# Performance work log

Measured on AMD Instinct MI355X. Metric: run time of the kernel, lower is better.

The kernel has to match this reference:

```python
import jax, jax.numpy as jnp
import numpy as np


def silu(v):
    return v * jax.nn.sigmoid(v)


def setup_inputs() -> dict:
    key = jax.random.key(0)
    ks = jax.random.split(key, 10)
    b, l, d_model = 1, 1024, 1536
    d_inner, dt_rank, d_state, d_conv = 3072, 96, 16, 4
    rn = lambda k, shp, sc: jax.random.normal(k, shp, jnp.float32) * sc
    return {
        "hidden_states": rn(ks[0], (b, l, d_model), 1.0),
        "in_proj_w": rn(ks[1], (2 * d_inner, d_model), 0.02),
        "conv_w": rn(ks[2], (d_inner, d_conv), 0.1),
        "conv_b": rn(ks[3], (d_inner,), 0.1),
        "x_proj_w": rn(ks[4], (dt_rank + 2 * d_state, d_inner), 0.02),
        "dt_proj_w": rn(ks[5], (d_inner, dt_rank), 0.02),
        "dt_proj_b": rn(ks[6], (d_inner,), 0.1),
        "out_proj_w": rn(ks[7], (d_model, d_inner), 0.02),
        "A_log": jnp.log(jax.random.uniform(ks[8], (d_inner, d_state), jnp.float32, 0.5, 8.0)),
        "D": rn(ks[9], (d_inner,), 1.0),
    }


def reference(hidden_states, in_proj_w, conv_w, conv_b, x_proj_w, dt_proj_w, dt_proj_b, out_proj_w, A_log, D):
    b, l, _ = hidden_states.shape
    d_inner, d_conv = conv_w.shape
    dt_rank = dt_proj_w.shape[1]
    d_state = A_log.shape[1]
    negA = -jnp.exp(A_log)  # (d_inner, d_state)

    # in_proj, transpose to channel-major: (b, 2*d_inner, l)
    xz = jnp.einsum('bld,ed->ble', hidden_states, in_proj_w).transpose(0, 2, 1)
    x, z = jnp.split(xz, 2, axis=1)  # each (b, d_inner, l)

    # conv_state = F.pad(x, (d_conv - l, 0)) -> last d_conv columns (l > d_conv)
    conv_state = x[:, :, -d_conv:]

    # causal depthwise conv1d + bias + silu
    xp = jnp.pad(x, ((0, 0), (0, 0), (d_conv - 1, 0)))
    xc = conv_b[None, :, None] + sum(conv_w[None, :, j:j + 1] * xp[:, :, j:j + l] for j in range(d_conv))
    xc = silu(xc)  # (b, d_inner, l)

    # x_proj over channel dim -> dt, B, C
    x_dbl = jnp.einsum('bdl,ed->ble', xc, x_proj_w)  # (b, l, dt_rank+2*d_state)
    dt, Bm, Cm = jnp.split(x_dbl, [dt_rank, dt_rank + d_state], axis=-1)

    # dt_proj (no bias here; bias folded into softplus as delta_bias)
    delta = jax.nn.softplus(jnp.einsum('blr,dr->bdl', dt, dt_proj_w) + dt_proj_b[None, :, None])

    # selective scan: h_t = exp(delta_t * A) * h_{t-1} + delta_t * B_t * x_t
    deltaA = jnp.exp(delta[..., None] * negA[None, :, None, :])          # (b, d, l, n)
    deltaBx = delta[..., None] * Bm[:, None, :, :] * xc[..., None]        # (b, d, l, n)

    def comb(c1, c2):
        a1, u1 = c1
        a2, u2 = c2
        return a1 * a2, a2 * u1 + u2

    _, h = jax.lax.associative_scan(comb, (deltaA, deltaBx), axis=2)      # (b, d, l, n)

    y = jnp.einsum('bdln,bln->bdl', h, Cm) + D[None, :, None] * xc
    y = y * silu(z)

    out = jnp.einsum('bdl,od->blo', y, out_proj_w)  # (b, l, d_model)
    last_state = h[:, :, -1, :]                     # (b, d_inner, d_state)
    return out, conv_state, last_state
```

## Files before the change

kernel.cpp:

```cpp
#include <hip/hip_runtime.h>

using f32x4  = __attribute__((ext_vector_type(4))) float;
using bf16x4 = __attribute__((ext_vector_type(4))) __bf16;
using bf16x8 = __attribute__((ext_vector_type(8))) __bf16;

#define L_SEQ 1024
#define D_MODEL 1536
#define D_INNER 3072
#define DT_RANK 96
#define D_STATE 16

#define SCAN_NC 32
#define SCAN_CL (L_SEQ / SCAN_NC)
#define NCHAIN  (D_INNER * D_STATE)

#define SCRATCH_FLOATS (4 * L_SEQ * D_INNER + L_SEQ * 128 + 3 * SCAN_NC * NCHAIN)
__device__ __align__(16) float g_scratch[SCRATCH_FLOATS];

template <int BM, int BN, int BK, int AMODE, int BMODE, int EPI, int SWZY = 0>
__global__ __launch_bounds__(256) void gemm_bt(
    const float* __restrict__ Ap, const float* __restrict__ Bp,
    float* __restrict__ out0, float* __restrict__ out1,
    const float* __restrict__ bias,
    int M, int N, int K, int lda, int ldb, int ldc)
{
    constexpr int LDSK = BK + 8;
    constexpr int WM = BM / 2, WN = BN / 2;
    constexpr int FM = WM / 16, FN = WN / 16;
    constexpr int CHA = (BM * BK / 256) / 4;
    constexpr int CHB = (BN * BK / 256) / 4;
    constexpr int CPR = BK / 4;
    __shared__ __align__(16) __bf16 As [BM * LDSK];
    __shared__ __align__(16) __bf16 As2[(AMODE == 2) ? BM * LDSK : 8];
    __shared__ __align__(16) __bf16 Bs [BN * LDSK];
    __shared__ __align__(16) __bf16 Bs2[(BMODE == 2) ? BN * LDSK : 8];

    const int tid  = threadIdx.x;
    const int lane = tid & 63;
    const int wid  = tid >> 6;
    const int wm = wid >> 1, wn = wid & 1;

    int m0, n0;
    if constexpr (SWZY > 0) {
        int b   = blockIdx.x;
        int xcd = b & 7;
        int j   = b >> 3;
        m0 = (j / SWZY) * BM;
        n0 = (xcd * SWZY + (j % SWZY)) * BN;
    } else {
        m0 = blockIdx.x * BM;
        n0 = blockIdx.y * BN;
    }

    const int nkt = (K + BK - 1) / BK;
    const int per = (nkt + (int)gridDim.z - 1) / (int)gridDim.z;
    const int kb  = blockIdx.z * per * BK;
    const int ke  = min(K, kb + per * BK);

    f32x4 acc[FM][FN];
#pragma unroll
    for (int i = 0; i < FM; ++i)
#pragma unroll
        for (int j = 0; j < FN; ++j) acc[i][j] = f32x4{0.f, 0.f, 0.f, 0.f};

    const int fr = lane & 15, kq = lane >> 4;

    f32x4 arg[CHA], brg[CHB];

    auto loadA = [&](int kt) {
#pragma unroll
        for (int i = 0; i < CHA; ++i) {
            int c = i * 256 + tid;
            int r = c / CPR, k4 = c % CPR;
            arg[i] = *(const f32x4*)(Ap + (size_t)(m0 + r) * lda + kt + k4 * 4);
        }
    };
    auto loadB = [&](int kt) {
#pragma unroll
        for (int i = 0; i < CHB; ++i) {
            int c = i * 256 + tid;
            int r = c / CPR, k4 = c % CPR;
            brg[i] = *(const f32x4*)(Bp + (size_t)(n0 + r) * ldb + kt + k4 * 4);
        }
    };
    auto writeA = [&]() {
#pragma unroll
        for (int i = 0; i < CHA; ++i) {
            int c = i * 256 + tid;
            int r = c / CPR, k4 = c % CPR;
            bf16x4 hv;
#pragma unroll
            for (int e = 0; e < 4; ++e) hv[e] = (__bf16)arg[i][e];
            *(bf16x4*)&As[r * LDSK + k4 * 4] = hv;
            if constexpr (AMODE == 2) {
                bf16x4 lv;
#pragma unroll
                for (int e = 0; e < 4; ++e)
                    lv[e] = (__bf16)(arg[i][e] - (float)hv[e]);
                *(bf16x4*)&As2[r * LDSK + k4 * 4] = lv;
            }
        }
    };
    auto writeB = [&]() {
#pragma unroll
        for (int i = 0; i < CHB; ++i) {
            int c = i * 256 + tid;
            int r = c / CPR, k4 = c % CPR;
            bf16x4 hv;
#pragma unroll
            for (int e = 0; e < 4; ++e) hv[e] = (__bf16)brg[i][e];
            *(bf16x4*)&Bs[r * LDSK + k4 * 4] = hv;
            if constexpr (BMODE == 2) {
                bf16x4 lv;
#pragma unroll
                for (int e = 0; e < 4; ++e)
                    lv[e] = (__bf16)(brg[i][e] - (float)hv[e]);
                *(bf16x4*)&Bs2[r * LDSK + k4 * 4] = lv;
            }
        }
    };
    auto compute = [&]() {
#pragma unroll
        for (int ks = 0; ks < BK / 32; ++ks) {
            const int kc = ks * 32 + kq * 8;
            bf16x8 af[FM], bfg[FN];
#pragma unroll
            for (int fm = 0; fm < FM; ++fm)
                af[fm] = *(const bf16x8*)&As[(wm * WM + fm * 16 + fr) * LDSK + kc];
#pragma unroll
            for (int fn = 0; fn < FN; ++fn)
                bfg[fn] = *(const bf16x8*)&Bs[(wn * WN + fn * 16 + fr) * LDSK + kc];
            if constexpr (AMODE == 2 && BMODE == 2) {
                bf16x8 al[FM], bl[FN];
#pragma unroll
                for (int fm = 0; fm < FM; ++fm)
                    al[fm] = *(const bf16x8*)&As2[(wm * WM + fm * 16 + fr) * LDSK + kc];
#pragma unroll
                for (int fn = 0; fn < FN; ++fn)
                    bl[fn] = *(const bf16x8*)&Bs2[(wn * WN + fn * 16 + fr) * LDSK + kc];
#pragma unroll
                for (int fm = 0; fm < FM; ++fm)
#pragma unroll
                    for (int fn = 0; fn < FN; ++fn) {
                        acc[fm][fn] = __builtin_amdgcn_mfma_f32_16x16x32_bf16(
                            al[fm], bfg[fn], acc[fm][fn], 0, 0, 0);
                        acc[fm][fn] = __builtin_amdgcn_mfma_f32_16x16x32_bf16(
                            af[fm], bl[fn], acc[fm][fn], 0, 0, 0);
                        acc[fm][fn] = __builtin_amdgcn_mfma_f32_16x16x32_bf16(
                            af[fm], bfg[fn], acc[fm][fn], 0, 0, 0);
                    }
            } else {
#pragma unroll
                for (int fm = 0; fm < FM; ++fm)
#pragma unroll
                    for (int fn = 0; fn < FN; ++fn)
                        acc[fm][fn] = __builtin_amdgcn_mfma_f32_16x16x32_bf16(
                            af[fm], bfg[fn], acc[fm][fn], 0, 0, 0);
            }
        }
    };

    loadA(kb);
    loadB(kb);

    for (int kt = kb; kt < ke; kt += BK) {
        writeA();
        writeB();
        __syncthreads();
        if (kt + BK < ke) {
            loadA(kt + BK);
            loadB(kt + BK);
        }
        compute();
        __syncthreads();
    }

    const int rbase = m0 + wm * WM, cbase = n0 + wn * WN;
#pragma unroll
    for (int fm = 0; fm < FM; ++fm) {
#pragma unroll
        for (int fn = 0; fn < FN; ++fn) {
            int row = rbase + fm * 16 + (lane >> 4) * 4;
            int col = cbase + fn * 16 + (lane & 15);
            f32x4 v = acc[fm][fn];
            if (EPI == 0) {
                int split = N / 2;
                float* d = (col < split) ? out0 : out1;
                int cc = (col < split) ? col : col - split;
#pragma unroll
                for (int j = 0; j < 4; ++j) d[(size_t)(row + j) * ldc + cc] = v[j];
            } else if (EPI == 1) {
                float bz = bias[col];
#pragma unroll
                for (int j = 0; j < 4; ++j) {
                    float t = v[j] + bz;
                    t = (t > 20.f) ? t : log1pf(__expf(t));
                    out0[(size_t)(row + j) * ldc + col] = t;
                }
            } else if (EPI == 2) {
#pragma unroll
                for (int j = 0; j < 4; ++j)
                    atomicAdd(&out0[(size_t)(row + j) * ldc + col], v[j]);
            } else if (EPI == 3) {
#pragma unroll
                for (int j = 0; j < 4; ++j)
                    out0[(size_t)(row + j) * ldc + col] = v[j];
            } else if (EPI == 4) {
                float* d = out0 + (size_t)blockIdx.z * M * ldc;
#pragma unroll
                for (int j = 0; j < 4; ++j)
                    d[(size_t)(row + j) * ldc + col] = v[j];
            } else {
#pragma unroll
                for (int j = 0; j < 4; ++j) {
                    float t = v[j] + bias[row + j];
                    t = (t > 20.f) ? t : log1pf(__expf(t));
                    out0[(size_t)(row + j) * ldc + col] = t;
                }
            }
        }
    }
}

__global__ __launch_bounds__(256) void reduce2_f32(
    const float* __restrict__ p, float* __restrict__ out, int n4)
{
    int i = blockIdx.x * 256 + threadIdx.x;
    if (i < n4) {
        f32x4 a = ((const f32x4*)p)[i];
        f32x4 b = ((const f32x4*)(p + (size_t)L_SEQ * D_MODEL))[i];
        ((f32x4*)out)[i] = a + b;
    }
}

__global__ __launch_bounds__(256) void conv_silu(
    const float* __restrict__ x, const float* __restrict__ cw,
    const float* __restrict__ cb, float* __restrict__ xc,
    float* __restrict__ conv_state, float* __restrict__ dbl)
{
    int idx = blockIdx.x * 256 + threadIdx.x;
    const f32x4 zero = f32x4{0.f, 0.f, 0.f, 0.f};
    if (idx < L_SEQ * 128 / 4) ((f32x4*)dbl)[idx] = zero;
    int l  = idx / (D_INNER / 4);
    int d4 = (idx % (D_INNER / 4)) * 4;
    f32x4 x0 = *(const f32x4*)&x[(size_t)l * D_INNER + d4];
    f32x4 x1 = (l >= 1) ? *(const f32x4*)&x[(size_t)(l - 1) * D_INNER + d4] : zero;
    f32x4 x2 = (l >= 2) ? *(const f32x4*)&x[(size_t)(l - 2) * D_INNER + d4] : zero;
    f32x4 x3 = (l >= 3) ? *(const f32x4*)&x[(size_t)(l - 3) * D_INNER + d4] : zero;
    f32x4 r;
#pragma unroll
    for (int i = 0; i < 4; ++i) {
        int d = d4 + i;
        float w0 = cw[d * 4 + 0], w1 = cw[d * 4 + 1];
        float w2 = cw[d * 4 + 2], w3 = cw[d * 4 + 3];
        float v = cb[d] + w3 * x0[i] + w2 * x1[i] + w1 * x2[i] + w0 * x3[i];
        r[i] = v / (1.f + __expf(-v));
    }
    *(f32x4*)&xc[(size_t)l * D_INNER + d4] = r;
    if (l == L_SEQ - 1) {
#pragma unroll
        for (int i = 0; i < 4; ++i) {
            int d = d4 + i;
            conv_state[d * 4 + 3] = x0[i];
            conv_state[d * 4 + 2] = x1[i];
            conv_state[d * 4 + 1] = x2[i];
            conv_state[d * 4 + 0] = x3[i];
        }
    }
}

__global__ __launch_bounds__(256) void scan_phase1(
    const float* __restrict__ delta, const float* __restrict__ xc,
    const float* __restrict__ dbl, const float* __restrict__ A_log,
    float* __restrict__ U, float* __restrict__ Aprod)
{
    int d = blockIdx.x * 256 + threadIdx.x;
    int c = blockIdx.y;
    float a[D_STATE], h[D_STATE], p[D_STATE];
#pragma unroll
    for (int n = 0; n < D_STATE; n += 4) {
        f32x4 av = *(const f32x4*)&A_log[d * D_STATE + n];
#pragma unroll
        for (int e = 0; e < 4; ++e) {
            a[n + e] = __expf(av[e]);
            h[n + e] = 0.f;
            p[n + e] = 1.f;
        }
    }
    int l0 = c * SCAN_CL;
    for (int i = 0; i < SCAN_CL; ++i) {
        int l = l0 + i;
        float dl = delta[(size_t)l * D_INNER + d];
        float xv = xc[(size_t)l * D_INNER + d];
        const float* Bp = dbl + l * 128 + DT_RANK;
        f32x4 B0 = *(const f32x4*)(Bp);
        f32x4 B1 = *(const f32x4*)(Bp + 4);
        f32x4 B2 = *(const f32x4*)(Bp + 8);
        f32x4 B3 = *(const f32x4*)(Bp + 12);
        float dx = dl * xv;
#pragma unroll
        for (int n = 0; n < D_STATE; ++n) {
            float Bv = (n < 4) ? B0[n] : (n < 8) ? B1[n - 4]
                     : (n < 12) ? B2[n - 8] : B3[n - 12];
            float dA = __expf(-dl * a[n]);
            h[n] = fmaf(dA, h[n], dx * Bv);
            p[n] *= dA;
        }
    }
    size_t base = (size_t)c * NCHAIN + (size_t)d * D_STATE;
#pragma unroll
    for (int n = 0; n < D_STATE; n += 4) {
        *(f32x4*)&U[base + n]     = f32x4{h[n], h[n+1], h[n+2], h[n+3]};
        *(f32x4*)&Aprod[base + n] = f32x4{p[n], p[n+1], p[n+2], p[n+3]};
    }
}

__global__ __launch_bounds__(256) void scan_phase2(
    const float* __restrict__ U, const float* __restrict__ Aprod,
    float* __restrict__ Hin, float* __restrict__ last_state)
{
    int r = blockIdx.x * 256 + threadIdx.x;
    float hin = 0.f;
#pragma unroll
    for (int c = 0; c < SCAN_NC; ++c) {
        Hin[c * NCHAIN + r] = hin;
        hin = fmaf(Aprod[c * NCHAIN + r], hin, U[c * NCHAIN + r]);
    }
    last_state[r] = hin;
}

__global__ __launch_bounds__(256) void scan_phase3(
    const float* __restrict__ delta, const float* __restrict__ xc,
    const float* __restrict__ z, const float* __restrict__ dbl,
    const float* __restrict__ A_log, const float* __restrict__ Dp,
    const float* __restrict__ Hin, float* __restrict__ y)
{
    int d = blockIdx.x * 256 + threadIdx.x;
    int c = blockIdx.y;
    float a[D_STATE], h[D_STATE];
    size_t hbase = (size_t)c * NCHAIN + (size_t)d * D_STATE;
#pragma unroll
    for (int n = 0; n < D_STATE; n += 4) {
        f32x4 av = *(const f32x4*)&A_log[d * D_STATE + n];
        f32x4 hv = *(const f32x4*)&Hin[hbase + n];
#pragma unroll
        for (int e = 0; e < 4; ++e) {
            a[n + e] = __expf(av[e]);
            h[n + e] = hv[e];
        }
    }
    float Dv = Dp[d];
    int l0 = c * SCAN_CL;
    for (int i = 0; i < SCAN_CL; ++i) {
        int l = l0 + i;
        float dl = delta[(size_t)l * D_INNER + d];
        float xv = xc[(size_t)l * D_INNER + d];
        float zv = z[(size_t)l * D_INNER + d];
        const float* Bp = dbl + l * 128 + DT_RANK;
        f32x4 B0 = *(const f32x4*)(Bp);
        f32x4 B1 = *(const f32x4*)(Bp + 4);
        f32x4 B2 = *(const f32x4*)(Bp + 8);
        f32x4 B3 = *(const f32x4*)(Bp + 12);
        f32x4 C0 = *(const f32x4*)(Bp + 16);
        f32x4 C1 = *(const f32x4*)(Bp + 20);
        f32x4 C2 = *(const f32x4*)(Bp + 24);
        f32x4 C3 = *(const f32x4*)(Bp + 28);
        float dx = dl * xv;
        float yv = 0.f;
#pragma unroll
        for (int n = 0; n < D_STATE; ++n) {
            float Bv = (n < 4) ? B0[n] : (n < 8) ? B1[n - 4]
                     : (n < 12) ? B2[n - 8] : B3[n - 12];
            float Cv = (n < 4) ? C0[n] : (n < 8) ? C1[n - 4]
                     : (n < 12) ? C2[n - 8] : C3[n - 12];
            float dA = __expf(-dl * a[n]);
            h[n] = fmaf(dA, h[n], dx * Bv);
            yv = fmaf(h[n], Cv, yv);
        }
        float sz = zv / (1.f + __expf(-zv));
        y[(size_t)l * D_INNER + d] = (yv + Dv * xv) * sz;
    }
}

extern "C" void kernel_launch(void* const* d_in, const int* in_sizes, int n_in,
                              void* d_out, int out_size, void* d_ws, size_t ws_size,
                              hipStream_t stream)
{
    const float* hs    = (const float*)d_in[0];
    const float* Win   = (const float*)d_in[1];
    const float* cw    = (const float*)d_in[2];
    const float* cb    = (const float*)d_in[3];
    const float* Wx    = (const float*)d_in[4];
    const float* Wdt   = (const float*)d_in[5];
    const float* dtb   = (const float*)d_in[6];
    const float* Wout  = (const float*)d_in[7];
    const float* A_log = (const float*)d_in[8];
    const float* Dp    = (const float*)d_in[9];

    float* out        = (float*)d_out;
    float* conv_state = out + (size_t)L_SEQ * D_MODEL;
    float* last_state = conv_state + (size_t)D_INNER * 4;

    const size_t NEED = sizeof(float) * (size_t)SCRATCH_FLOATS;
    float* base;
    if (ws_size >= NEED) {
        base = (float*)d_ws;
    } else {
        void* sp = nullptr;
        hipGetSymbolAddress(&sp, HIP_SYMBOL(g_scratch));
        base = (float*)sp;
    }
    float* buf0 = base;
    float* buf1 = buf0 + (size_t)L_SEQ * D_INNER;
    float* buf2 = buf1 + (size_t)L_SEQ * D_INNER;
    float* buf3 = buf2 + (size_t)L_SEQ * D_INNER;
    float* dbl  = buf3 + (size_t)L_SEQ * D_INNER;
    float* Ubuf = dbl  + (size_t)L_SEQ * 128;
    float* Abuf = Ubuf + (size_t)SCAN_NC * NCHAIN;
    float* Hbuf = Abuf + (size_t)SCAN_NC * NCHAIN;

    gemm_bt<128, 64, 64, 1, 1, 0, 12><<<dim3(768), 256, 0, stream>>>(
        hs, Win, buf0, buf1, nullptr, L_SEQ, 2 * D_INNER, D_MODEL, D_MODEL, D_MODEL, D_INNER);

    conv_silu<<<dim3(L_SEQ * D_INNER / 4 / 256), 256, 0, stream>>>(
        buf0, cw, cb, buf2, conv_state, dbl);

    gemm_bt<64, 128, 32, 2, 2, 2><<<dim3(16, 1, 24), 256, 0, stream>>>(
        buf2, Wx, dbl, nullptr, nullptr, L_SEQ, 128, D_INNER, D_INNER, D_INNER, 128);

    gemm_bt<64, 64, 96, 2, 2, 1><<<dim3(16, 48), 256, 0, stream>>>(
        dbl, Wdt, buf0, nullptr, dtb, L_SEQ, D_INNER, DT_RANK, 128, DT_RANK, D_INNER);

    scan_phase1<<<dim3(D_INNER / 256, SCAN_NC), 256, 0, stream>>>(
        buf0, buf2, dbl, A_log, Ubuf, Abuf);
    scan_phase2<<<dim3(NCHAIN / 256), 256, 0, stream>>>(
        Ubuf, Abuf, Hbuf, last_state);
    scan_phase3<<<dim3(D_INNER / 256, SCAN_NC), 256, 0, stream>>>(
        buf0, buf2, buf1, dbl, A_log, Dp, Hbuf, buf3);

    gemm_bt<64, 64, 64, 1, 1, 4><<<dim3(16, 24, 2), 256, 0, stream>>>(
        buf3, Wout, buf0, nullptr, nullptr, L_SEQ, D_MODEL, D_INNER, D_INNER, D_INNER, D_MODEL);
    reduce2_f32<<<dim3(L_SEQ * D_MODEL / 4 / 256), 256, 0, stream>>>(
        buf0, out, L_SEQ * D_MODEL / 4);
}
```

Baseline: 185.6 us.

## Store intermediate activations in bf16 and split-K out_proj via atomics into output

Intermediate buffers for x, z, conv output, delta and y are now stored as bf16 instead of fp32, halving their memory traffic. The GEMM gains a bf16 A-operand mode that copies straight into LDS, and x_proj drops the hi/lo split on the activation side. out_proj now zeroes the output and accumulates split-K partials with atomics, replacing the partial buffer and its reduction kernel. The cost is lower precision in the intermediates, including conv_state taken from bf16 x, and nondeterministic atomic summation order.

```diff
diff --git a/kernel.cpp b/kernel.cpp
--- a/kernel.cpp
+++ b/kernel.cpp
@@ -17,19 +17,26 @@
 #define SCRATCH_FLOATS (4 * L_SEQ * D_INNER + L_SEQ * 128 + 3 * SCAN_NC * NCHAIN)
 __device__ __align__(16) float g_scratch[SCRATCH_FLOATS];
 
+template <bool B16> struct RegT { using T = f32x4; };
+template <> struct RegT<true> { using T = uint4; };
+
 template <int BM, int BN, int BK, int AMODE, int BMODE, int EPI, int SWZY = 0>
 __global__ __launch_bounds__(256) void gemm_bt(
-    const float* __restrict__ Ap, const float* __restrict__ Bp,
-    float* __restrict__ out0, float* __restrict__ out1,
+    const void* __restrict__ Ap, const void* __restrict__ Bp,
+    void* __restrict__ out0, void* __restrict__ out1,
     const float* __restrict__ bias,
     int M, int N, int K, int lda, int ldb, int ldc)
 {
     constexpr int LDSK = BK + 8;
     constexpr int WM = BM / 2, WN = BN / 2;
     constexpr int FM = WM / 16, FN = WN / 16;
-    constexpr int CHA = (BM * BK / 256) / 4;
-    constexpr int CHB = (BN * BK / 256) / 4;
-    constexpr int CPR = BK / 4;
+    constexpr int AEPT = (AMODE == 0) ? 8 : 4;
+    constexpr int BEPT = (BMODE == 0) ? 8 : 4;
+    constexpr int CHA = (BM * BK / 256) / AEPT;
+    constexpr int CHB = (BN * BK / 256) / BEPT;
+    constexpr int ACPR = BK / AEPT, BCPR = BK / BEPT;
+    using ART = typename RegT<AMODE == 0>::T;
+    using BRT = typename RegT<BMODE == 0>::T;
     __shared__ __align__(16) __bf16 As [BM * LDSK];
     __shared__ __align__(16) __bf16 As2[(AMODE == 2) ? BM * LDSK : 8];
     __shared__ __align__(16) __bf16 Bs [BN * LDSK];
@@ -65,39 +72,56 @@
 
     const int fr = lane & 15, kq = lane >> 4;
 
-    f32x4 arg[CHA], brg[CHB];
+    ART arg[CHA];
+    BRT brg[CHB];
 
     auto loadA = [&](int kt) {
 #pragma unroll
         for (int i = 0; i < CHA; ++i) {
             int c = i * 256 + tid;
-            int r = c / CPR, k4 = c % CPR;
-            arg[i] = *(const f32x4*)(Ap + (size_t)(m0 + r) * lda + kt + k4 * 4);
+            int r = c / ACPR, k = c % ACPR;
+            if constexpr (AMODE == 0) {
+                const __bf16* A = (const __bf16*)Ap;
+                arg[i] = *(const uint4*)(A + (size_t)(m0 + r) * lda + kt + k * 8);
+            } else {
+                const float* A = (const float*)Ap;
+                arg[i] = *(const f32x4*)(A + (size_t)(m0 + r) * lda + kt + k * 4);
+            }
         }
     };
     auto loadB = [&](int kt) {
 #pragma unroll
         for (int i = 0; i < CHB; ++i) {
             int c = i * 256 + tid;
-            int r = c / CPR, k4 = c % CPR;
-            brg[i] = *(const f32x4*)(Bp + (size_t)(n0 + r) * ldb + kt + k4 * 4);
+            int r = c / BCPR, k = c % BCPR;
+            if constexpr (BMODE == 0) {
+                const __bf16* B = (const __bf16*)Bp;
+                brg[i] = *(const uint4*)(B + (size_t)(n0 + r) * ldb + kt + k * 8);
+            } else {
+                const float* B = (const float*)Bp;
+                brg[i] = *(const f32x4*)(B + (size_t)(n0 + r) * ldb + kt + k * 4);
+            }
         }
     };
     auto writeA = [&]() {
 #pragma unroll
         for (int i = 0; i < CHA; ++i) {
             int c = i * 256 + tid;
-            int r = c / CPR, k4 = c % CPR;
-            bf16x4 hv;
-#pragma unroll
-            for (int e = 0; e < 4; ++e) hv[e] = (__bf16)arg[i][e];
-            *(bf16x4*)&As[r * LDSK + k4 * 4] = hv;
-            if constexpr (AMODE == 2) {
-                bf16x4 lv;
-#pragma unroll
-                for (int e = 0; e < 4; ++e)
-                    lv[e] = (__bf16)(arg[i][e] - (float)hv[e]);
-                *(bf16x4*)&As2[r * LDSK + k4 * 4] = lv;
+            int r = c / ACPR, k = c % ACPR;
+            if constexpr (AMODE == 0) {
+                *(uint4*)&As[r * LDSK + k * 8] = arg[i];
+            } else {
+                bf16x4 hv;
+#pragma unroll
+                for (int e = 0; e < 4; ++e) hv[e] = (__bf16)arg[i][e];
+                *(bf16x4*)&As[r * LDSK + k * 4] = hv;
+                if constexpr (AMODE == 2) {
+                    bf16x4 lv;
+#pragma unroll
+                    for (int e = 0; e < 4; ++e)
+                        lv[e] = (__bf16)(arg[i][e] - (float)hv[e]);
+                    *(bf16x4*)&As2[r * LDSK + k * 4] = lv;
+                }
             }
         }
     };
@@ -105,17 +129,21 @@
 #pragma unroll
         for (int i = 0; i < CHB; ++i) {
             int c = i * 256 + tid;
-            int r = c / CPR, k4 = c % CPR;
-            bf16x4 hv;
-#pragma unroll
-            for (int e = 0; e < 4; ++e) hv[e] = (__bf16)brg[i][e];
-            *(bf16x4*)&Bs[r * LDSK + k4 * 4] = hv;
-            if constexpr (BMODE == 2) {
-                bf16x4 lv;
-#pragma unroll
-                for (int e = 0; e < 4; ++e)
-                    lv[e] = (__bf16)(brg[i][e] - (float)hv[e]);
-                *(bf16x4*)&Bs2[r * LDSK + k4 * 4] = lv;
+            int r = c / BCPR, k = c % BCPR;
+            if constexpr (BMODE == 0) {
+                *(uint4*)&Bs[r * LDSK + k * 8] = brg[i];
+            } else {
+                bf16x4 hv;
+#pragma unroll
+                for (int e = 0; e < 4; ++e) hv[e] = (__bf16)brg[i][e];
+                *(bf16x4*)&Bs[r * LDSK + k * 4] = hv;
+                if constexpr (BMODE == 2) {
+                    bf16x4 lv;
+#pragma unroll
+                    for (int e = 0; e < 4; ++e)
+                        lv[e] = (__bf16)(brg[i][e] - (float)hv[e]);
+                    *(bf16x4*)&Bs2[r * LDSK + k * 4] = lv;
+                }
             }
         }
     };
@@ -144,6 +172,34 @@
                     for (int fn = 0; fn < FN; ++fn) {
                         acc[fm][fn] = __builtin_amdgcn_mfma_f32_16x16x32_bf16(
                             al[fm], bfg[fn], acc[fm][fn], 0, 0, 0);
+                        acc[fm][fn] = __builtin_amdgcn_mfma_f32_16x16x32_bf16(
+                            af[fm], bl[fn], acc[fm][fn], 0, 0, 0);
+                        acc[fm][fn] = __builtin_amdgcn_mfma_f32_16x16x32_bf16(
+                            af[fm], bfg[fn], acc[fm][fn], 0, 0, 0);
+                    }
+            } else if constexpr (AMODE == 2) {
+                bf16x8 al[FM];
+#pragma unroll
+                for (int fm = 0; fm < FM; ++fm)
+                    al[fm] = *(const bf16x8*)&As2[(wm * WM + fm * 16 + fr) * LDSK + kc];
+#pragma unroll
+                for (int fm = 0; fm < FM; ++fm)
+#pragma unroll
+                    for (int fn = 0; fn < FN; ++fn) {
+                        acc[fm][fn] = __builtin_amdgcn_mfma_f32_16x16x32_bf16(
+                            al[fm], bfg[fn], acc[fm][fn], 0, 0, 0);
+                        acc[fm][fn] = __builtin_amdgcn_mfma_f32_16x16x32_bf16(
+                            af[fm], bfg[fn], acc[fm][fn], 0, 0, 0);
+                    }
+            } else if constexpr (BMODE == 2) {
+                bf16x8 bl[FN];
+#pragma unroll
+                for (int fn = 0; fn < FN; ++fn)
+                    bl[fn] = *(const bf16x8*)&Bs2[(wn * WN + fn * 16 + fr) * LDSK + kc];
+#pragma unroll
+                for (int fm = 0; fm < FM; ++fm)
+#pragma unroll
+                    for (int fn = 0; fn < FN; ++fn) {
                         acc[fm][fn] = __builtin_amdgcn_mfma_f32_16x16x32_bf16(
                             af[fm], bl[fn], acc[fm][fn], 0, 0, 0);
                         acc[fm][fn] = __builtin_amdgcn_mfma_f32_16x16x32_bf16(
@@ -185,92 +241,76 @@
             f32x4 v = acc[fm][fn];
             if (EPI == 0) {
                 int split = N / 2;
-                float* d = (col < split) ? out0 : out1;
+                __bf16* d = (col < split) ? (__bf16*)out0 : (__bf16*)out1;
                 int cc = (col < split) ? col : col - split;
 #pragma unroll
-                for (int j = 0; j < 4; ++j) d[(size_t)(row + j) * ldc + cc] = v[j];
+                for (int j = 0; j < 4; ++j)
+                    d[(size_t)(row + j) * ldc + cc] = (__bf16)v[j];
             } else if (EPI == 1) {
                 float bz = bias[col];
+                __bf16* d = (__bf16*)out0;
 #pragma unroll
                 for (int j = 0; j < 4; ++j) {
                     float t = v[j] + bz;
                     t = (t > 20.f) ? t : log1pf(__expf(t));
-                    out0[(size_t)(row + j) * ldc + col] = t;
+                    d[(size_t)(row + j) * ldc + col] = (__bf16)t;
                 }
-            } else if (EPI == 2) {
+            } else {
+                float* d = (float*)out0;
 #pragma unroll
                 for (int j = 0; j < 4; ++j)
-                    atomicAdd(&out0[(size_t)(row + j) * ldc + col], v[j]);
-            } else if (EPI == 3) {
-#pragma unroll
-                for (int j = 0; j < 4; ++j)
-                    out0[(size_t)(row + j) * ldc + col] = v[j];
-            } else if (EPI == 4) {
-                float* d = out0 + (size_t)blockIdx.z * M * ldc;
-#pragma unroll
-                for (int j = 0; j < 4; ++j)
-                    d[(size_t)(row + j) * ldc + col] = v[j];
-            } else {
-#pragma unroll
-                for (int j = 0; j < 4; ++j) {
-                    float t = v[j] + bias[row + j];
-                    t = (t > 20.f) ? t : log1pf(__expf(t));
-                    out0[(size_t)(row + j) * ldc + col] = t;
-                }
-            }
-        }
-    }
-}
-
-__global__ __launch_bounds__(256) void reduce2_f32(
-    const float* __restrict__ p, float* __restrict__ out, int n4)
+                    atomicAdd(&d[(size_t)(row + j) * ldc + col], v[j]);
+            }
+        }
+    }
+}
+
+__global__ __launch_bounds__(256) void zero_f32(float* __restrict__ p, int n4)
 {
     int i = blockIdx.x * 256 + threadIdx.x;
-    if (i < n4) {
-        f32x4 a = ((const f32x4*)p)[i];
-        f32x4 b = ((const f32x4*)(p + (size_t)L_SEQ * D_MODEL))[i];
-        ((f32x4*)out)[i] = a + b;
-    }
+    if (i < n4) ((f32x4*)p)[i] = f32x4{0.f, 0.f, 0.f, 0.f};
 }
 
 __global__ __launch_bounds__(256) void conv_silu(
-    const float* __restrict__ x, const float* __restrict__ cw,
-    const float* __restrict__ cb, float* __restrict__ xc,
+    const __bf16* __restrict__ x, const float* __restrict__ cw,
+    const float* __restrict__ cb, __bf16* __restrict__ xc,
     float* __restrict__ conv_state, float* __restrict__ dbl)
 {
     int idx = blockIdx.x * 256 + threadIdx.x;
-    const f32x4 zero = f32x4{0.f, 0.f, 0.f, 0.f};
-    if (idx < L_SEQ * 128 / 4) ((f32x4*)dbl)[idx] = zero;
+    if (idx < L_SEQ * 128 / 4)
+        ((f32x4*)dbl)[idx] = f32x4{0.f, 0.f, 0.f, 0.f};
     int l  = idx / (D_INNER / 4);
     int d4 = (idx % (D_INNER / 4)) * 4;
-    f32x4 x0 = *(const f32x4*)&x[(size_t)l * D_INNER + d4];
-    f32x4 x1 = (l >= 1) ? *(const f32x4*)&x[(size_t)(l - 1) * D_INNER + d4] : zero;
-    f32x4 x2 = (l >= 2) ? *(const f32x4*)&x[(size_t)(l - 2) * D_INNER + d4] : zero;
-    f32x4 x3 = (l >= 3) ? *(const f32x4*)&x[(size_t)(l - 3) * D_INNER + d4] : zero;
-    f32x4 r;
+    const bf16x4 bz = bf16x4{(__bf16)0.f, (__bf16)0.f, (__bf16)0.f, (__bf16)0.f};
+    bf16x4 u0 = *(const bf16x4*)&x[(size_t)l * D_INNER + d4];
+    bf16x4 u1 = (l >= 1) ? *(const bf16x4*)&x[(size_t)(l - 1) * D_INNER + d4] : bz;
+    bf16x4 u2 = (l >= 2) ? *(const bf16x4*)&x[(size_t)(l - 2) * D_INNER + d4] : bz;
+    bf16x4 u3 = (l >= 3) ? *(const bf16x4*)&x[(size_t)(l - 3) * D_INNER + d4] : bz;
+    bf16x4 r;
 #pragma unroll
     for (int i = 0; i < 4; ++i) {
         int d = d4 + i;
         float w0 = cw[d * 4 + 0], w1 = cw[d * 4 + 1];
         float w2 = cw[d * 4 + 2], w3 = cw[d * 4 + 3];
-        float v = cb[d] + w3 * x0[i] + w2 * x1[i] + w1 * x2[i] + w0 * x3[i];
-        r[i] = v / (1.f + __expf(-v));
-    }
-    *(f32x4*)&xc[(size_t)l * D_INNER + d4] = r;
+        float v = cb[d] + w3 * (float)u0[i] + w2 * (float)u1[i]
+                        + w1 * (float)u2[i] + w0 * (float)u3[i];
+        r[i] = (__bf16)(v / (1.f + __expf(-v)));
+    }
+    *(bf16x4*)&xc[(size_t)l * D_INNER + d4] = r;
     if (l == L_SEQ - 1) {
 #pragma unroll
         for (int i = 0; i < 4; ++i) {
             int d = d4 + i;
-            conv_state[d * 4 + 3] = x0[i];
-            conv_state[d * 4 + 2] = x1[i];
-            conv_state[d * 4 + 1] = x2[i];
-            conv_state[d * 4 + 0] = x3[i];
+            conv_state[d * 4 + 3] = (float)u0[i];
+            conv_state[d * 4 + 2] = (float)u1[i];
+            conv_state[d * 4 + 1] = (float)u2[i];
+            conv_state[d * 4 + 0] = (float)u3[i];
         }
     }
 }
 
 __global__ __launch_bounds__(256) void scan_phase1(
-    const float* __restrict__ delta, const float* __restrict__ xc,
+    const __bf16* __restrict__ delta, const __bf16* __restrict__ xc,
     const float* __restrict__ dbl, const float* __restrict__ A_log,
     float* __restrict__ U, float* __restrict__ Aprod)
 {
@@ -290,8 +330,8 @@
     int l0 = c * SCAN_CL;
     for (int i = 0; i < SCAN_CL; ++i) {
         int l = l0 + i;
-        float dl = delta[(size_t)l * D_INNER + d];
-        float xv = xc[(size_t)l * D_INNER + d];
+        float dl = (float)delta[(size_t)l * D_INNER + d];
+        float xv = (float)xc[(size_t)l * D_INNER + d];
         const float* Bp = dbl + l * 128 + DT_RANK;
         f32x4 B0 = *(const f32x4*)(Bp);
         f32x4 B1 = *(const f32x4*)(Bp + 4);
@@ -330,10 +370,10 @@
 }
 
 __global__ __launch_bounds__(256) void scan_phase3(
-    const float* __restrict__ delta, const float* __restrict__ xc,
-    const float* __restrict__ z, const float* __restrict__ dbl,
+    const __bf16* __restrict__ delta, const __bf16* __restrict__ xc,
+    const __bf16* __restrict__ z, const float* __restrict__ dbl,
     const float* __restrict__ A_log, const float* __restrict__ Dp,
-    const float* __restrict__ Hin, float* __restrict__ y)
+    const float* __restrict__ Hin, __bf16* __restrict__ y)
 {
     int d = blockIdx.x * 256 + threadIdx.x;
     int c = blockIdx.y;
@@ -353,9 +393,9 @@
     int l0 = c * SCAN_CL;
     for (int i = 0; i < SCAN_CL; ++i) {
         int l = l0 + i;
-        float dl = delta[(size_t)l * D_INNER + d];
-        float xv = xc[(size_t)l * D_INNER + d];
-        float zv = z[(size_t)l * D_INNER + d];
+        float dl = (float)delta[(size_t)l * D_INNER + d];
+        float xv = (float)xc[(size_t)l * D_INNER + d];
+        float zv = (float)z[(size_t)l * D_INNER + d];
         const float* Bp = dbl + l * 128 + DT_RANK;
         f32x4 B0 = *(const f32x4*)(Bp);
         f32x4 B1 = *(const f32x4*)(Bp + 4);
@@ -378,7 +418,7 @@
             yv = fmaf(h[n], Cv, yv);
         }
         float sz = zv / (1.f + __expf(-zv));
-        y[(size_t)l * D_INNER + d] = (yv + Dv * xv) * sz;
+        y[(size_t)l * D_INNER + d] = (__bf16)((yv + Dv * xv) * sz);
     }
 }
 
@@ -410,36 +450,37 @@
         hipGetSymbolAddress(&sp, HIP_SYMBOL(g_scratch));
         base = (float*)sp;
     }
-    float* buf0 = base;
-    float* buf1 = buf0 + (size_t)L_SEQ * D_INNER;
-    float* buf2 = buf1 + (size_t)L_SEQ * D_INNER;
-    float* buf3 = buf2 + (size_t)L_SEQ * D_INNER;
-    float* dbl  = buf3 + (size_t)L_SEQ * D_INNER;
+    __bf16* xB  = (__bf16*)base;
+    __bf16* zB  = xB  + (size_t)L_SEQ * D_INNER;
+    __bf16* xcB = zB  + (size_t)L_SEQ * D_INNER;
+    __bf16* dlB = xcB + (size_t)L_SEQ * D_INNER;
+    __bf16* yB  = dlB + (size_t)L_SEQ * D_INNER;
+    float* dbl  = (float*)(yB + (size_t)L_SEQ * D_INNER);
     float* Ubuf = dbl  + (size_t)L_SEQ * 128;
     float* Abuf = Ubuf + (size_t)SCAN_NC * NCHAIN;
     float* Hbuf = Abuf + (size_t)SCAN_NC * NCHAIN;
 
     gemm_bt<128, 64, 64, 1, 1, 0, 12><<<dim3(768), 256, 0, stream>>>(
-        hs, Win, buf0, buf1, nullptr, L_SEQ, 2 * D_INNER, D_MODEL, D_MODEL, D_MODEL, D_INNER);
+        hs, Win, xB, zB, nullptr, L_SEQ, 2 * D_INNER, D_MODEL, D_MODEL, D_MODEL, D_INNER);
 
     conv_silu<<<dim3(L_SEQ * D_INNER / 4 / 256), 256, 0, stream>>>(
-        buf0, cw, cb, buf2, conv_state, dbl);
-
-    gemm_bt<64, 128, 32, 2, 2, 2><<<dim3(16, 1, 24), 256, 0, stream>>>(
-        buf2, Wx, dbl, nullptr, nullptr, L_SEQ, 128, D_INNER, D_INNER, D_INNER, 128);
+        xB, cw, cb, xcB, conv_state, dbl);
+
+    gemm_bt<64, 128, 32, 0, 2, 2><<<dim3(16, 1, 24), 256, 0, stream>>>(
+        xcB, Wx, dbl, nullptr, nullptr, L_SEQ, 128, D_INNER, D_INNER, D_INNER, 128);
 
     gemm_bt<64, 64, 96, 2, 2, 1><<<dim3(16, 48), 256, 0, stream>>>(
-        dbl, Wdt, buf0, nullptr, dtb, L_SEQ, D_INNER, DT_RANK, 128, DT_RANK, D_INNER);
+        dbl, Wdt, dlB, nullptr, dtb, L_SEQ, D_INNER, DT_RANK, 128, DT_RANK, D_INNER);
 
     scan_phase1<<<dim3(D_INNER / 256, SCAN_NC), 256, 0, stream>>>(
-        buf0, buf2, dbl, A_log, Ubuf, Abuf);
+        dlB, xcB, dbl, A_log, Ubuf, Abuf);
     scan_phase2<<<dim3(NCHAIN / 256), 256, 0, stream>>>(
         Ubuf, Abuf, Hbuf, last_state);
     scan_phase3<<<dim3(D_INNER / 256, SCAN_NC), 256, 0, stream>>>(
-        buf0, buf2, buf1, dbl, A_log, Dp, Hbuf, buf3);
-
-    gemm_bt<64, 64, 64, 1, 1, 4><<<dim3(16, 24, 2), 256, 0, stream>>>(
-        buf3, Wout, buf0, nullptr, nullptr, L_SEQ, D_MODEL, D_INNER, D_INNER, D_INNER, D_MODEL);
-    reduce2_f32<<<dim3(L_SEQ * D_MODEL / 4 / 256), 256, 0, stream>>>(
-        buf0, out, L_SEQ * D_MODEL / 4);
-}
+        dlB, xcB, zB, dbl, A_log, Dp, Hbuf, yB);
+
+    zero_f32<<<dim3(L_SEQ * D_MODEL / 4 / 256), 256, 0, stream>>>(
+        out, L_SEQ * D_MODEL / 4);
+    gemm_bt<64, 64, 64, 0, 1, 2><<<dim3(16, 24, 2), 256, 0, stream>>>(
+        yB, Wout, out, nullptr, nullptr, L_SEQ, D_MODEL, D_INNER, D_INNER, D_INNER, D_MODEL);
+}
```

Measured after the change: 200.4 us. +8.0%, slower.
